# Optimization experiments

Measured on AMD Instinct MI355X. Metric: run time of the kernel, lower is better.

Reference implementation:

```python
import jax, jax.numpy as jnp
import numpy as np


def setup_inputs() -> dict:
    key = jax.random.key(0)
    k1, k2, k3, k4, k5 = jax.random.split(key, 5)
    B, S, F = 16384, 8192, 512
    inputs = jax.random.normal(k1, (B, F), dtype=jnp.float32)
    support_vectors = jax.random.normal(k2, (S, F), dtype=jnp.float32)
    coefficients = jax.random.uniform(k3, (1, S), dtype=jnp.float32)
    rho = jax.random.uniform(k4, (1,), dtype=jnp.float32)
    # small positive gamma typical of RBF kernels on normalized features
    gamma = jax.random.uniform(k5, (), dtype=jnp.float32) * jnp.float32(0.01)
    return {"inputs": inputs, "support_vectors": support_vectors,
            "coefficients": coefficients, "rho": rho, "gamma": gamma}


def reference(inputs, support_vectors, coefficients, rho, gamma):
    # (same math as the broadcast-subtract-square-sum in the original,
    #  without materializing the [B, S, F] intermediate)
    x_sq = jnp.sum(inputs * inputs, axis=1, keepdims=True)          # [B, 1]
    s_sq = jnp.sum(support_vectors * support_vectors, axis=1)       # [S]
    cross = inputs @ support_vectors.T                              # [B, S]
    d2 = x_sq + s_sq[None, :] - 2.0 * cross                         # [B, S]
    k = jnp.exp(-gamma * d2)                                        # [B, S]
    score = jnp.sum(k * coefficients, axis=1)                       # [B]
    return score - rho                                              # rho broadcasts [1] -> [B]
```

## Files before the change

kernel.cpp:

```cpp
#include <hip/hip_runtime.h>
#include <stdint.h>
#include <stddef.h>

#define BROWS  16384
#define SROWS  8192
#define FDIM   512
#define NCHUNK 4
#define SCHUNK (SROWS / NCHUNK)
#define BN     32
#define NTILES (SCHUNK / BN)
#define BM     256
#define KSTEPS (FDIM / 16)

#define LOG2E 1.44269504088896340736f

typedef __bf16 bf16x8 __attribute__((ext_vector_type(8)));
typedef float  f32x16 __attribute__((ext_vector_type(16)));

__device__ inline void gload16(const void* g, void* l) {
  __builtin_amdgcn_global_load_lds(
      (const __attribute__((address_space(1))) void*)g,
      (__attribute__((address_space(3))) void*)l, 16, 0, 0);
}

__global__ __launch_bounds__(256) void prep_s_kernel(
    const float* __restrict__ S, const float* __restrict__ coeff,
    const float* __restrict__ gamma, __bf16* __restrict__ Sb,
    float* __restrict__ c2)
{
  const int lane = threadIdx.x & 63;
  const int wid  = threadIdx.x >> 6;
  const int row  = (blockIdx.x << 2) + wid;
  const float* src = S + ((size_t)row << 9) + (lane << 3);
  float4 a = ((const float4*)src)[0];
  float4 b = ((const float4*)src)[1];
  float sq = a.x*a.x + a.y*a.y + a.z*a.z + a.w*a.w +
             b.x*b.x + b.y*b.y + b.z*b.z + b.w*b.w;
  bf16x8 v;
  v[0]=(__bf16)a.x; v[1]=(__bf16)a.y; v[2]=(__bf16)a.z; v[3]=(__bf16)a.w;
  v[4]=(__bf16)b.x; v[5]=(__bf16)b.y; v[6]=(__bf16)b.z; v[7]=(__bf16)b.w;
  *(bf16x8*)(Sb + ((size_t)row << 9) + (lane << 3)) = v;
  #pragma unroll
  for (int m = 1; m < 64; m <<= 1) sq += __shfl_xor(sq, m, 64);
  if (lane == 0) {
    float g = gamma[0];
    c2[row] = coeff[row] * exp2f(-g * LOG2E * sq);
  }
}

__global__ __launch_bounds__(512, 2) void ocsvm_main_kernel(
    const float* __restrict__ X, const __bf16* __restrict__ Sb,
    const float* __restrict__ c2, const float* __restrict__ gamma,
    float* __restrict__ partials)
{
  __shared__ char lds[65536];
  const int tid  = threadIdx.x;
  const int wid  = tid >> 6;
  const int lane = tid & 63;
  const int col  = lane & 31;
  const int half = lane >> 5;

  const int bx    = blockIdx.x;
  const int xcd   = bx & 7;
  const int grp   = bx >> 3;
  const int chunk = xcd >> 1;
  const int mtile = (grp << 1) + (xcd & 1);
  const int m0    = mtile * BM;
  const int chunk0 = chunk * SCHUNK;

  const float gam = gamma[0];
  const float K2  = 2.0f * gam * LOG2E;

  const int arow = m0 + (wid << 5) + col;
  const float* xp = X + ((size_t)arow << 9) + (half << 3);
  bf16x8 afrag[KSTEPS];
  float sq = 0.0f;
  #pragma unroll
  for (int ks = 0; ks < KSTEPS; ++ks) {
    float4 a = *(const float4*)(xp + (ks << 4));
    float4 b = *(const float4*)(xp + (ks << 4) + 4);
    sq += a.x*a.x + a.y*a.y + a.z*a.z + a.w*a.w +
          b.x*b.x + b.y*b.y + b.z*b.z + b.w*b.w;
    bf16x8 v;
    v[0]=(__bf16)a.x; v[1]=(__bf16)a.y; v[2]=(__bf16)a.z; v[3]=(__bf16)a.w;
    v[4]=(__bf16)b.x; v[5]=(__bf16)b.y; v[6]=(__bf16)b.z; v[7]=(__bf16)b.w;
    afrag[ks] = v;
  }
  sq += __shfl_xor(sq, 32, 64);
  const float e_x = exp2f(-gam * LOG2E * sq);

#define STAGE(bufsel, tile)                                                   \
  {                                                                           \
    _Pragma("unroll")                                                         \
    for (int r = 0; r < 4; ++r) {                                             \
      const int t_all = (r << 9) + tid;                                       \
      const int cs = t_all & 31;                                              \
      const int kb = t_all >> 5;                                              \
      const char* src = (const char*)Sb +                                     \
          (((size_t)(chunk0 + ((tile) << 5) + cs)) << 10) + (kb << 4);        \
      char* dst = &lds[((bufsel) << 15) + (((r << 9) + (wid << 6)) << 4)];    \
      gload16(src, dst);                                                      \
    }                                                                         \
  }

  STAGE(0, 0);
  __syncthreads();

  float scoreAcc[16];
  #pragma unroll
  for (int i = 0; i < 16; ++i) scoreAcc[i] = 0.0f;

  const char* bread0 = &lds[(half << 9) + (col << 4)];
  const float* c2p = c2 + chunk0 + col;

  for (int t = 0; t < NTILES; ++t) {
    if (t + 1 < NTILES) STAGE((t + 1) & 1, t + 1);

    const char* bb = bread0 + ((t & 1) << 15);
    f32x16 acc0 = {};
    f32x16 acc1 = {};
    #pragma unroll
    for (int ks = 0; ks < KSTEPS; ks += 2) {
      bf16x8 b0 = *(const bf16x8*)(bb + (ks << 10));
      bf16x8 b1 = *(const bf16x8*)(bb + ((ks + 1) << 10));
      acc0 = __builtin_amdgcn_mfma_f32_32x32x16_bf16(afrag[ks],     b0, acc0, 0, 0, 0);
      acc1 = __builtin_amdgcn_mfma_f32_32x32x16_bf16(afrag[ks + 1], b1, acc1, 0, 0, 0);
    }

    const float c2v = c2p[t << 5];
    #pragma unroll
    for (int r2 = 0; r2 < 16; ++r2)
      scoreAcc[r2] += c2v * exp2f(K2 * (acc0[r2] + acc1[r2]));

    __syncthreads();
  }

  #pragma unroll
  for (int r2 = 0; r2 < 16; ++r2) {
    float v = scoreAcc[r2];
    v += __shfl_xor(v, 1, 64);
    v += __shfl_xor(v, 2, 64);
    v += __shfl_xor(v, 4, 64);
    v += __shfl_xor(v, 8, 64);
    v += __shfl_xor(v, 16, 64);
    const int rloc = (r2 & 3) + ((r2 >> 2) << 3) + (half << 2);
    const float exr = __shfl(e_x, rloc, 64);
    if (col == 0)
      partials[chunk * BROWS + m0 + (wid << 5) + rloc] = exr * v;
  }
#undef STAGE
}

__global__ __launch_bounds__(256) void reduce_kernel(
    const float* __restrict__ partials, const float* __restrict__ rho,
    float* __restrict__ out)
{
  const int i = blockIdx.x * 256 + threadIdx.x;
  float s = partials[i] + partials[BROWS + i] +
            partials[2 * BROWS + i] + partials[3 * BROWS + i];
  out[i] = s - rho[0];
}

extern "C" void kernel_launch(void* const* d_in, const int* in_sizes, int n_in,
                              void* d_out, int out_size, void* d_ws, size_t ws_size,
                              hipStream_t stream) {
  const float* X     = (const float*)d_in[0];
  const float* S     = (const float*)d_in[1];
  const float* coeff = (const float*)d_in[2];
  const float* rho   = (const float*)d_in[3];
  const float* gamma = (const float*)d_in[4];
  float* out = (float*)d_out;

  char* ws = (char*)d_ws;
  __bf16* Sb      = (__bf16*)ws;
  float*  c2      = (float*)(ws + (size_t)SROWS * FDIM * 2);
  float*  parts   = (float*)(ws + (size_t)SROWS * FDIM * 2 + SROWS * 4);

  prep_s_kernel<<<SROWS / 4, 256, 0, stream>>>(S, coeff, gamma, Sb, c2);
  ocsvm_main_kernel<<<NCHUNK * 64, 512, 0, stream>>>(X, Sb, c2, gamma, parts);
  reduce_kernel<<<BROWS / 256, 256, 0, stream>>>(parts, rho, out);
}
```

Measured before the change: 162.1 us.

## Give each wave two 32-row A tiles and fold coefficient into exp exponent

Halves the block to 256 threads and has each wave own two 32-row slices of X, so each LDS-loaded B fragment feeds two MFMAs and LDS read traffic per FLOP drops. The per-support coefficient is precomputed as log2(coeff) minus the norm term and added inside the exponent via FMAs, with the raw hardware exp2 intrinsic replacing exp2f. The A-fragment load is moved after issuing the first stage to overlap it with the global load. This doubles register use for A fragments and accumulators, lowers occupancy to one block per CU with four waves, and log2f yields -inf when a coefficient is zero.

```diff
diff --git a/kernel.cpp b/kernel.cpp
--- a/kernel.cpp
+++ b/kernel.cpp
@@ -26,7 +26,7 @@
 __global__ __launch_bounds__(256) void prep_s_kernel(
     const float* __restrict__ S, const float* __restrict__ coeff,
     const float* __restrict__ gamma, __bf16* __restrict__ Sb,
-    float* __restrict__ c2)
+    float* __restrict__ lc2)
 {
   const int lane = threadIdx.x & 63;
   const int wid  = threadIdx.x >> 6;
@@ -44,13 +44,13 @@
   for (int m = 1; m < 64; m <<= 1) sq += __shfl_xor(sq, m, 64);
   if (lane == 0) {
     float g = gamma[0];
-    c2[row] = coeff[row] * exp2f(-g * LOG2E * sq);
-  }
-}
-
-__global__ __launch_bounds__(512, 2) void ocsvm_main_kernel(
+    lc2[row] = log2f(coeff[row]) - g * LOG2E * sq;
+  }
+}
+
+__global__ __launch_bounds__(256, 1) void ocsvm_main_kernel(
     const float* __restrict__ X, const __bf16* __restrict__ Sb,
-    const float* __restrict__ c2, const float* __restrict__ gamma,
+    const float* __restrict__ lc2, const float* __restrict__ gamma,
     float* __restrict__ partials)
 {
   __shared__ char lds[65536];
@@ -71,82 +71,103 @@
   const float gam = gamma[0];
   const float K2  = 2.0f * gam * LOG2E;
 
-  const int arow = m0 + (wid << 5) + col;
-  const float* xp = X + ((size_t)arow << 9) + (half << 3);
-  bf16x8 afrag[KSTEPS];
-  float sq = 0.0f;
-  #pragma unroll
-  for (int ks = 0; ks < KSTEPS; ++ks) {
-    float4 a = *(const float4*)(xp + (ks << 4));
-    float4 b = *(const float4*)(xp + (ks << 4) + 4);
-    sq += a.x*a.x + a.y*a.y + a.z*a.z + a.w*a.w +
-          b.x*b.x + b.y*b.y + b.z*b.z + b.w*b.w;
-    bf16x8 v;
-    v[0]=(__bf16)a.x; v[1]=(__bf16)a.y; v[2]=(__bf16)a.z; v[3]=(__bf16)a.w;
-    v[4]=(__bf16)b.x; v[5]=(__bf16)b.y; v[6]=(__bf16)b.z; v[7]=(__bf16)b.w;
-    afrag[ks] = v;
-  }
-  sq += __shfl_xor(sq, 32, 64);
-  const float e_x = exp2f(-gam * LOG2E * sq);
-
 #define STAGE(bufsel, tile)                                                   \
   {                                                                           \
     _Pragma("unroll")                                                         \
-    for (int r = 0; r < 4; ++r) {                                             \
-      const int t_all = (r << 9) + tid;                                       \
+    for (int r = 0; r < 8; ++r) {                                             \
+      const int t_all = (r << 8) + tid;                                       \
       const int cs = t_all & 31;                                              \
       const int kb = t_all >> 5;                                              \
       const char* src = (const char*)Sb +                                     \
           (((size_t)(chunk0 + ((tile) << 5) + cs)) << 10) + (kb << 4);        \
-      char* dst = &lds[((bufsel) << 15) + (((r << 9) + (wid << 6)) << 4)];    \
+      char* dst = &lds[((bufsel) << 15) + (((r << 8) + (wid << 6)) << 4)];    \
       gload16(src, dst);                                                      \
     }                                                                         \
   }
 
   STAGE(0, 0);
+
+  const float* xp0 = X + ((size_t)(m0 + (wid << 6) + col) << 9) + (half << 3);
+  const float* xp1 = xp0 + (32u << 9);
+  bf16x8 af0[KSTEPS], af1[KSTEPS];
+  float sq0 = 0.0f, sq1 = 0.0f;
+  #pragma unroll
+  for (int ks = 0; ks < KSTEPS; ++ks) {
+    float4 a = *(const float4*)(xp0 + (ks << 4));
+    float4 b = *(const float4*)(xp0 + (ks << 4) + 4);
+    sq0 += a.x*a.x + a.y*a.y + a.z*a.z + a.w*a.w +
+           b.x*b.x + b.y*b.y + b.z*b.z + b.w*b.w;
+    bf16x8 v;
+    v[0]=(__bf16)a.x; v[1]=(__bf16)a.y; v[2]=(__bf16)a.z; v[3]=(__bf16)a.w;
+    v[4]=(__bf16)b.x; v[5]=(__bf16)b.y; v[6]=(__bf16)b.z; v[7]=(__bf16)b.w;
+    af0[ks] = v;
+    float4 c = *(const float4*)(xp1 + (ks << 4));
+    float4 d = *(const float4*)(xp1 + (ks << 4) + 4);
+    sq1 += c.x*c.x + c.y*c.y + c.z*c.z + c.w*c.w +
+           d.x*d.x + d.y*d.y + d.z*d.z + d.w*d.w;
+    bf16x8 w;
+    w[0]=(__bf16)c.x; w[1]=(__bf16)c.y; w[2]=(__bf16)c.z; w[3]=(__bf16)c.w;
+    w[4]=(__bf16)d.x; w[5]=(__bf16)d.y; w[6]=(__bf16)d.z; w[7]=(__bf16)d.w;
+    af1[ks] = w;
+  }
+  sq0 += __shfl_xor(sq0, 32, 64);
+  sq1 += __shfl_xor(sq1, 32, 64);
+  const float e_x0 = __builtin_amdgcn_exp2f(-gam * LOG2E * sq0);
+  const float e_x1 = __builtin_amdgcn_exp2f(-gam * LOG2E * sq1);
+
   __syncthreads();
 
-  float scoreAcc[16];
-  #pragma unroll
-  for (int i = 0; i < 16; ++i) scoreAcc[i] = 0.0f;
+  float score0[16], score1[16];
+  #pragma unroll
+  for (int i = 0; i < 16; ++i) { score0[i] = 0.0f; score1[i] = 0.0f; }
 
   const char* bread0 = &lds[(half << 9) + (col << 4)];
-  const float* c2p = c2 + chunk0 + col;
+  const float* lc2p = lc2 + chunk0 + col;
 
   for (int t = 0; t < NTILES; ++t) {
     if (t + 1 < NTILES) STAGE((t + 1) & 1, t + 1);
 
     const char* bb = bread0 + ((t & 1) << 15);
-    f32x16 acc0 = {};
-    f32x16 acc1 = {};
+    f32x16 acc00 = {}, acc01 = {}, acc10 = {}, acc11 = {};
     #pragma unroll
     for (int ks = 0; ks < KSTEPS; ks += 2) {
       bf16x8 b0 = *(const bf16x8*)(bb + (ks << 10));
       bf16x8 b1 = *(const bf16x8*)(bb + ((ks + 1) << 10));
-      acc0 = __builtin_amdgcn_mfma_f32_32x32x16_bf16(afrag[ks],     b0, acc0, 0, 0, 0);
-      acc1 = __builtin_amdgcn_mfma_f32_32x32x16_bf16(afrag[ks + 1], b1, acc1, 0, 0, 0);
-    }
-
-    const float c2v = c2p[t << 5];
+      acc00 = __builtin_amdgcn_mfma_f32_32x32x16_bf16(af0[ks],     b0, acc00, 0, 0, 0);
+      acc10 = __builtin_amdgcn_mfma_f32_32x32x16_bf16(af1[ks],     b0, acc10, 0, 0, 0);
+      acc01 = __builtin_amdgcn_mfma_f32_32x32x16_bf16(af0[ks + 1], b1, acc01, 0, 0, 0);
+      acc11 = __builtin_amdgcn_mfma_f32_32x32x16_bf16(af1[ks + 1], b1, acc11, 0, 0, 0);
+    }
+
+    const float lc2v = lc2p[t << 5];
     #pragma unroll
-    for (int r2 = 0; r2 < 16; ++r2)
-      scoreAcc[r2] += c2v * exp2f(K2 * (acc0[r2] + acc1[r2]));
+    for (int r2 = 0; r2 < 16; ++r2) {
+      score0[r2] += __builtin_amdgcn_exp2f(
+          __builtin_fmaf(K2, acc00[r2], __builtin_fmaf(K2, acc01[r2], lc2v)));
+      score1[r2] += __builtin_amdgcn_exp2f(
+          __builtin_fmaf(K2, acc10[r2], __builtin_fmaf(K2, acc11[r2], lc2v)));
+    }
 
     __syncthreads();
   }
 
   #pragma unroll
   for (int r2 = 0; r2 < 16; ++r2) {
-    float v = scoreAcc[r2];
-    v += __shfl_xor(v, 1, 64);
-    v += __shfl_xor(v, 2, 64);
-    v += __shfl_xor(v, 4, 64);
-    v += __shfl_xor(v, 8, 64);
-    v += __shfl_xor(v, 16, 64);
+    float v0 = score0[r2];
+    float v1 = score1[r2];
+    #pragma unroll
+    for (int m = 1; m < 32; m <<= 1) {
+      v0 += __shfl_xor(v0, m, 64);
+      v1 += __shfl_xor(v1, m, 64);
+    }
     const int rloc = (r2 & 3) + ((r2 >> 2) << 3) + (half << 2);
-    const float exr = __shfl(e_x, rloc, 64);
-    if (col == 0)
-      partials[chunk * BROWS + m0 + (wid << 5) + rloc] = exr * v;
+    const float ex0 = __shfl(e_x0, rloc, 64);
+    const float ex1 = __shfl(e_x1, rloc, 64);
+    if (col == 0) {
+      float* dst = partials + chunk * BROWS + m0 + (wid << 6);
+      dst[rloc]      = ex0 * v0;
+      dst[32 + rloc] = ex1 * v1;
+    }
   }
 #undef STAGE
 }
@@ -172,11 +193,11 @@
   float* out = (float*)d_out;
 
   char* ws = (char*)d_ws;
-  __bf16* Sb      = (__bf16*)ws;
-  float*  c2      = (float*)(ws + (size_t)SROWS * FDIM * 2);
-  float*  parts   = (float*)(ws + (size_t)SROWS * FDIM * 2 + SROWS * 4);
-
-  prep_s_kernel<<<SROWS / 4, 256, 0, stream>>>(S, coeff, gamma, Sb, c2);
-  ocsvm_main_kernel<<<NCHUNK * 64, 512, 0, stream>>>(X, Sb, c2, gamma, parts);
+  __bf16* Sb    = (__bf16*)ws;
+  float*  lc2   = (float*)(ws + (size_t)SROWS * FDIM * 2);
+  float*  parts = (float*)(ws + (size_t)SROWS * FDIM * 2 + SROWS * 4);
+
+  prep_s_kernel<<<SROWS / 4, 256, 0, stream>>>(S, coeff, gamma, Sb, lc2);
+  ocsvm_main_kernel<<<NCHUNK * 64, 256, 0, stream>>>(X, Sb, lc2, gamma, parts);
   reduce_kernel<<<BROWS / 256, 256, 0, stream>>>(parts, rho, out);
 }
```

New measurement: 178.4 us. +10.1%, slower.

## Triple-buffer support tiles with one barrier and fold coefficient into exponent

Applied to the files above, without the earlier changes.

Switches the LDS staging of support-vector tiles from double to triple buffering and replaces the two __syncthreads per tile with explicit vmcnt waits plus a single barrier. The first tile's load is also issued before the X fragment conversion so the two overlap. The coefficient multiply is folded into the exponent as a log2 term computed in the prep kernel, and the per-element exp uses fma plus the raw hardware exp2. The LDS footprint grows to 96KB per block, which may limit occupancy to fewer blocks per CU, and log2 of the coefficients fails for zero or negative values.

```diff
diff --git a/kernel.cpp b/kernel.cpp
--- a/kernel.cpp
+++ b/kernel.cpp
@@ -26,7 +26,7 @@
 __global__ __launch_bounds__(256) void prep_s_kernel(
     const float* __restrict__ S, const float* __restrict__ coeff,
     const float* __restrict__ gamma, __bf16* __restrict__ Sb,
-    float* __restrict__ c2)
+    float* __restrict__ lc2)
 {
   const int lane = threadIdx.x & 63;
   const int wid  = threadIdx.x >> 6;
@@ -44,16 +44,16 @@
   for (int m = 1; m < 64; m <<= 1) sq += __shfl_xor(sq, m, 64);
   if (lane == 0) {
     float g = gamma[0];
-    c2[row] = coeff[row] * exp2f(-g * LOG2E * sq);
+    lc2[row] = log2f(coeff[row]) - g * LOG2E * sq;
   }
 }
 
 __global__ __launch_bounds__(512, 2) void ocsvm_main_kernel(
     const float* __restrict__ X, const __bf16* __restrict__ Sb,
-    const float* __restrict__ c2, const float* __restrict__ gamma,
+    const float* __restrict__ lc2, const float* __restrict__ gamma,
     float* __restrict__ partials)
 {
-  __shared__ char lds[65536];
+  __shared__ char lds[98304];
   const int tid  = threadIdx.x;
   const int wid  = tid >> 6;
   const int lane = tid & 63;
@@ -71,6 +71,22 @@
   const float gam = gamma[0];
   const float K2  = 2.0f * gam * LOG2E;
 
+#define STAGE(bufsel, tile)                                                   \
+  {                                                                           \
+    _Pragma("unroll")                                                         \
+    for (int r = 0; r < 4; ++r) {                                             \
+      const int t_all = (r << 9) + tid;                                       \
+      const int cs = t_all & 31;                                              \
+      const int kb = t_all >> 5;                                              \
+      const char* src = (const char*)Sb +                                     \
+          (((size_t)(chunk0 + ((tile) << 5) + cs)) << 10) + (kb << 4);        \
+      char* dst = &lds[(bufsel) * 32768 + (((r << 9) + (wid << 6)) << 4)];    \
+      gload16(src, dst);                                                      \
+    }                                                                         \
+  }
+
+  STAGE(0, 0);
+
   const int arow = m0 + (wid << 5) + col;
   const float* xp = X + ((size_t)arow << 9) + (half << 3);
   bf16x8 afrag[KSTEPS];
@@ -87,36 +103,28 @@
     afrag[ks] = v;
   }
   sq += __shfl_xor(sq, 32, 64);
-  const float e_x = exp2f(-gam * LOG2E * sq);
-
-#define STAGE(bufsel, tile)                                                   \
-  {                                                                           \
-    _Pragma("unroll")                                                         \
-    for (int r = 0; r < 4; ++r) {                                             \
-      const int t_all = (r << 9) + tid;                                       \
-      const int cs = t_all & 31;                                              \
-      const int kb = t_all >> 5;                                              \
-      const char* src = (const char*)Sb +                                     \
-          (((size_t)(chunk0 + ((tile) << 5) + cs)) << 10) + (kb << 4);        \
-      char* dst = &lds[((bufsel) << 15) + (((r << 9) + (wid << 6)) << 4)];    \
-      gload16(src, dst);                                                      \
-    }                                                                         \
-  }
-
-  STAGE(0, 0);
-  __syncthreads();
+  const float e_x = __builtin_amdgcn_exp2f(-gam * LOG2E * sq);
 
   float scoreAcc[16];
   #pragma unroll
   for (int i = 0; i < 16; ++i) scoreAcc[i] = 0.0f;
 
   const char* bread0 = &lds[(half << 9) + (col << 4)];
-  const float* c2p = c2 + chunk0 + col;
+  const float* lc2p = lc2 + chunk0 + col;
 
+  int cur = 0;
   for (int t = 0; t < NTILES; ++t) {
-    if (t + 1 < NTILES) STAGE((t + 1) & 1, t + 1);
+    int nxt = cur + 1; if (nxt == 3) nxt = 0;
+    if (t + 1 < NTILES) {
+      STAGE(nxt, t + 1);
+      asm volatile("s_waitcnt vmcnt(4)" ::: "memory");
+    } else {
+      asm volatile("s_waitcnt vmcnt(0)" ::: "memory");
+    }
+    __builtin_amdgcn_s_barrier();
+    asm volatile("" ::: "memory");
 
-    const char* bb = bread0 + ((t & 1) << 15);
+    const char* bb = bread0 + cur * 32768;
     f32x16 acc0 = {};
     f32x16 acc1 = {};
     #pragma unroll
@@ -127,12 +135,13 @@
       acc1 = __builtin_amdgcn_mfma_f32_32x32x16_bf16(afrag[ks + 1], b1, acc1, 0, 0, 0);
     }
 
-    const float c2v = c2p[t << 5];
+    const float lc2v = lc2p[t << 5];
     #pragma unroll
-    for (int r2 = 0; r2 < 16; ++r2)
-      scoreAcc[r2] += c2v * exp2f(K2 * (acc0[r2] + acc1[r2]));
-
-    __syncthreads();
+    for (int r2 = 0; r2 < 16; ++r2) {
+      scoreAcc[r2] += __builtin_amdgcn_exp2f(
+          __builtin_fmaf(K2, acc0[r2], __builtin_fmaf(K2, acc1[r2], lc2v)));
+    }
+    cur = nxt;
   }
 
   #pragma unroll
@@ -172,11 +181,11 @@
   float* out = (float*)d_out;
 
   char* ws = (char*)d_ws;
-  __bf16* Sb      = (__bf16*)ws;
-  float*  c2      = (float*)(ws + (size_t)SROWS * FDIM * 2);
-  float*  parts   = (float*)(ws + (size_t)SROWS * FDIM * 2 + SROWS * 4);
+  __bf16* Sb    = (__bf16*)ws;
+  float*  lc2   = (float*)(ws + (size_t)SROWS * FDIM * 2);
+  float*  parts = (float*)(ws + (size_t)SROWS * FDIM * 2 + SROWS * 4);
 
-  prep_s_kernel<<<SROWS / 4, 256, 0, stream>>>(S, coeff, gamma, Sb, c2);
-  ocsvm_main_kernel<<<NCHUNK * 64, 512, 0, stream>>>(X, Sb, c2, gamma, parts);
+  prep_s_kernel<<<SROWS / 4, 256, 0, stream>>>(S, coeff, gamma, Sb, lc2);
+  ocsvm_main_kernel<<<NCHUNK * 64, 512, 0, stream>>>(X, Sb, lc2, gamma, parts);
   reduce_kernel<<<BROWS / 256, 256, 0, stream>>>(parts, rho, out);
 }
```

Result: faster. 151.4 us (-6.6%).
